# Kernel optimization log

Hardware: AMD Instinct MI355X
Metric: run time of the kernel (lower is better)

The kernel has to match this reference:

```python
import jax, jax.numpy as jnp
import numpy as np

N_NODES = 50000

def setup_inputs() -> dict:
    key = jax.random.key(0)
    k1, k2, k3, k4, k5 = jax.random.split(key, 5)
    x = jax.random.normal(k1, (50000, 512), dtype=jnp.float32)
    edge_row = jax.random.randint(k2, (800000,), 0, N_NODES, dtype=jnp.int64)
    edge_col = jax.random.randint(k3, (800000,), 0, N_NODES, dtype=jnp.int64)
    edge_val = jax.random.uniform(k4, (800000,), dtype=jnp.float32)
    # init like torch: uniform(-stdv, stdv), stdv = 1/sqrt(out_features)
    stdv = 1.0 / np.sqrt(96.0)
    weight = jax.random.uniform(k5, (512, 96), minval=-stdv, maxval=stdv, dtype=jnp.float32)
    return {"x": x, "edge_row": edge_row, "edge_col": edge_col, "edge_val": edge_val, "weight": weight}

def reference(x, edge_row, edge_col, edge_val, weight):
    # support = X @ W  -- dense GEMM [N, F_in] x [F_in, F_out]
    support = x @ weight
    # sparse adjacency matmul: out[row] += val * support[col]
    msgs = edge_val[:, None] * support[edge_col]          # [E, F_out]
    out = jax.ops.segment_sum(msgs, edge_row, num_segments=N_NODES)
    # act = ReLU (module default); bias=False
    return jax.nn.relu(out)
```

## Files before the change

### kernel.cpp

```cpp
#include <hip/hip_runtime.h>

#define N_NODES 50000
#define F_IN    512
#define F_OUT   96
#define N_EDGES 800000

#define RPB    128
#define NBKT   391
#define CAP    2560
#define ECHUNK 4096
#define NCHUNK ((N_EDGES + ECHUNK - 1) / ECHUNK)
#define GEMM_BLOCKS ((N_NODES + 63) / 64)

typedef __attribute__((ext_vector_type(8))) short bf16x8;
typedef __attribute__((ext_vector_type(4))) float f32x4;

typedef const __attribute__((address_space(1))) void* gas_ptr;
typedef __attribute__((address_space(3))) void* las_ptr;

__device__ __forceinline__ void gload_lds16(const void* g, void* l) {
    __builtin_amdgcn_global_load_lds((gas_ptr)g, (las_ptr)l, 16, 0, 0);
}

__device__ __forceinline__ unsigned short f2bf(float f) {
    unsigned int u = __float_as_uint(f);
    unsigned int r = (u + 0x7FFFu + ((u >> 16) & 1u)) >> 16;
    return (unsigned short)r;
}
__device__ __forceinline__ float bf2f(unsigned short h) {
    return __uint_as_float(((unsigned int)h) << 16);
}

__global__ __launch_bounds__(256) void k_wcast(const float* __restrict__ w,
                                               unsigned short* __restrict__ wTp,
                                               int* __restrict__ bcnt) {
    if (blockIdx.x == 0) {
        const int t = threadIdx.x;
        bcnt[t] = 0;
        if (t < 144) bcnt[256 + t] = 0;
    }
    const int i = blockIdx.x * 256 + threadIdx.x;
    if (i < F_OUT * F_IN) {
        const int n  = i >> 9;
        const int k  = i & 511;
        const int p  = k >> 6;
        const int kk = k & 63;
        const int slot = kk ^ ((n & 7) << 3);
        wTp[p * (F_OUT * 64) + n * 64 + slot] = f2bf(w[(size_t)k * F_OUT + n]);
    }
}

__global__ __launch_bounds__(256) void k_fused(const float* __restrict__ x,
                                               const unsigned short* __restrict__ wTp,
                                               unsigned short* __restrict__ support,
                                               const int* __restrict__ erow,
                                               const int* __restrict__ ecol,
                                               const float* __restrict__ eval,
                                               int* __restrict__ bcnt,
                                               float2* __restrict__ bucket) {
    __shared__ __align__(16) char smem[49152];
    const int tid = threadIdx.x;

    if (blockIdx.x < NCHUNK) {
        int* hist  = (int*)smem;
        int* gbase = hist + 400;
        int* lcur  = gbase + 400;
        for (int i = tid; i < NBKT; i += 256) { hist[i] = 0; lcur[i] = 0; }
        __syncthreads();

        const int base = blockIdx.x * ECHUNK;
        const int n = min(ECHUNK, N_EDGES - base);

        for (int i = tid; i < n; i += 256)
            atomicAdd(&hist[erow[base + i] >> 7], 1);
        __syncthreads();

        for (int b = tid; b < NBKT; b += 256)
            gbase[b] = hist[b] ? atomicAdd(&bcnt[b], hist[b]) : 0;
        __syncthreads();

        for (int i = tid; i < n; i += 256) {
            const int r = erow[base + i];
            const int b = r >> 7;
            const int pos = gbase[b] + atomicAdd(&lcur[b], 1);
            if (pos >= 0 && pos < CAP)
                bucket[(size_t)b * CAP + pos] = make_float2(
                    __int_as_float(((r & 127) << 16) | ecol[base + i]),
                    eval[base + i]);
        }
        return;
    }

    unsigned short* sB = (unsigned short*)smem;

    const int lane = tid & 63;
    const int wave = tid >> 6;
    const int r0   = (blockIdx.x - NCHUNK) * 64;
    const int lr   = lane & 15;
    const int kg   = lane >> 4;

    int grow = r0 + wave * 16 + lr;
    if (grow > N_NODES - 1) grow = N_NODES - 1;
    const float* xrow = x + (size_t)grow * F_IN + kg * 8;

    f32x4 acc[6];
    #pragma unroll
    for (int t = 0; t < 6; ++t) acc[t] = (f32x4){0.f, 0.f, 0.f, 0.f};

    float4 ar[8][4];

    auto BSTAGE = [&](int half) {
        const unsigned short* src = wTp + (size_t)half * (4 * F_OUT * 64);
        #pragma unroll
        for (int i = 0; i < 12; ++i) {
            const int chunk = i * 256 + tid;
            gload_lds16(src + chunk * 8, sB + chunk * 8);
        }
    };
    auto XLOAD = [&](int p) {
        const float* b = xrow + p * 64;
        ar[p][0] = *reinterpret_cast<const float4*>(b);
        ar[p][1] = *reinterpret_cast<const float4*>(b + 4);
        ar[p][2] = *reinterpret_cast<const float4*>(b + 32);
        ar[p][3] = *reinterpret_cast<const float4*>(b + 36);
    };
    auto COMPUTE = [&](int p) {
        const char* bb = (const char*)(sB + (p & 3) * (F_OUT * 64));
        #pragma unroll
        for (int ks = 0; ks < 2; ++ks) {
            const float4 a0 = ar[p][ks * 2];
            const float4 a1 = ar[p][ks * 2 + 1];
            bf16x8 af;
            af[0] = (short)f2bf(a0.x); af[1] = (short)f2bf(a0.y);
            af[2] = (short)f2bf(a0.z); af[3] = (short)f2bf(a0.w);
            af[4] = (short)f2bf(a1.x); af[5] = (short)f2bf(a1.y);
            af[6] = (short)f2bf(a1.z); af[7] = (short)f2bf(a1.w);
            #pragma unroll
            for (int t = 0; t < 6; ++t) {
                const int n    = t * 16 + lr;
                const int boff = (ks * 64 + kg * 16) ^ ((n & 7) << 4);
                const bf16x8 bfr = *reinterpret_cast<const bf16x8*>(bb + n * 128 + boff);
                acc[t] = __builtin_amdgcn_mfma_f32_16x16x32_bf16(af, bfr, acc[t], 0, 0, 0);
            }
        }
    };

    BSTAGE(0);
    __syncthreads();
    XLOAD(0); XLOAD(1); XLOAD(2);
    COMPUTE(0); XLOAD(3);
    COMPUTE(1); XLOAD(4);
    COMPUTE(2); XLOAD(5);
    COMPUTE(3);
    __syncthreads();
    BSTAGE(1);
    __syncthreads();
    XLOAD(6);
    COMPUTE(4); XLOAD(7);
    COMPUTE(5);
    COMPUTE(6);
    COMPUTE(7);

    #pragma unroll
    for (int t = 0; t < 6; ++t) {
        #pragma unroll
        for (int r = 0; r < 4; ++r) {
            const int row = r0 + wave * 16 + kg * 4 + r;
            if (row < N_NODES)
                support[(size_t)row * F_OUT + t * 16 + lr] = f2bf(acc[t][r]);
        }
    }
}

__global__ __launch_bounds__(256) void kS_sort(const int* __restrict__ bcnt,
                                               const float2* __restrict__ bucket,
                                               float2* __restrict__ bucket2,
                                               int* __restrict__ rowOffs) {
    __shared__ int cnt[RPB];
    __shared__ int sc[RPB];
    __shared__ int rbase[RPB];
    __shared__ int rcur[RPB];
    const int b   = blockIdx.x;
    const int tid = threadIdx.x;

    if (tid < RPB) { cnt[tid] = 0; rcur[tid] = 0; }
    __syncthreads();

    const int beg = b * CAP;
    const int n   = min(bcnt[b], CAP);

    for (int i = tid; i < n; i += 256)
        atomicAdd(&cnt[(__float_as_int(bucket[beg + i].x) >> 16) & 127], 1);
    __syncthreads();

    if (tid < RPB) sc[tid] = cnt[tid];
    __syncthreads();
    #pragma unroll
    for (int off = 1; off < RPB; off <<= 1) {
        int a = 0;
        if (tid < RPB && tid >= off) a = sc[tid - off];
        __syncthreads();
        if (tid < RPB) sc[tid] += a;
        __syncthreads();
    }
    if (tid < RPB) {
        const int rb = beg + sc[tid] - cnt[tid];
        rbase[tid] = rb;
        rowOffs[b * 129 + tid] = rb;
    }
    if (tid == RPB) rowOffs[b * 129 + RPB] = beg + n;
    __syncthreads();

    for (int i = tid; i < n; i += 256) {
        const float2 ev  = bucket[beg + i];
        const int    key = __float_as_int(ev.x);
        const int    r   = (key >> 16) & 127;
        const int    pos = rbase[r] + atomicAdd(&rcur[r], 1);
        bucket2[pos] = make_float2(__int_as_float(key & 0xFFFF), ev.y);
    }
}

__global__ __launch_bounds__(256) void k_gather(const int* __restrict__ rowOffs,
                                                const float2* __restrict__ bucket2,
                                                const unsigned short* __restrict__ support,
                                                float* __restrict__ out) {
    const int gid = blockIdx.x * 256 + threadIdx.x;
    if (gid >= N_NODES * 6) return;
    const int r   = gid / 6;
    const int f16 = gid - r * 6;

    const int idx = (r >> 7) * 129 + (r & 127);
    const int beg = rowOffs[idx];
    const int end = rowOffs[idx + 1];

    float acc[16];
    #pragma unroll
    for (int j = 0; j < 16; ++j) acc[j] = 0.f;

    for (int i = beg; i < end; ++i) {
        const float2 cv = bucket2[i];
        const int   c = __float_as_int(cv.x);
        const float v = cv.y;
        const unsigned short* sp = support + (size_t)c * F_OUT + f16 * 16;
        const bf16x8 s0 = *reinterpret_cast<const bf16x8*>(sp);
        const bf16x8 s1 = *reinterpret_cast<const bf16x8*>(sp + 8);
        #pragma unroll
        for (int j = 0; j < 8; ++j) {
            acc[j]     = fmaf(v, bf2f((unsigned short)s0[j]), acc[j]);
            acc[8 + j] = fmaf(v, bf2f((unsigned short)s1[j]), acc[8 + j]);
        }
    }

    float* o = out + (size_t)r * F_OUT + f16 * 16;
    #pragma unroll
    for (int q = 0; q < 4; ++q) {
        float4 ov;
        ov.x = fmaxf(acc[q * 4 + 0], 0.f);
        ov.y = fmaxf(acc[q * 4 + 1], 0.f);
        ov.z = fmaxf(acc[q * 4 + 2], 0.f);
        ov.w = fmaxf(acc[q * 4 + 3], 0.f);
        *reinterpret_cast<float4*>(o + q * 4) = ov;
    }
}

extern "C" void kernel_launch(void* const* d_in, const int* in_sizes, int n_in,
                              void* d_out, int out_size, void* d_ws, size_t ws_size,
                              hipStream_t stream) {
    const float* x    = (const float*)d_in[0];
    const int*   erow = (const int*)d_in[1];
    const int*   ecol = (const int*)d_in[2];
    const float* eval = (const float*)d_in[3];
    const float* w    = (const float*)d_in[4];
    float*       out  = (float*)d_out;

    unsigned short* support = (unsigned short*)d_ws;
    int*    bcnt    = (int*)((char*)d_ws + 9600000);
    int*    rowOffs = bcnt + 400;
    unsigned short* wTp = (unsigned short*)(rowOffs + 50560);
    float2* bucket  = (float2*)((char*)wTp + 98304);
    float2* bucket2 = bucket + (size_t)NBKT * CAP;

    k_wcast<<<(F_OUT * F_IN + 255) / 256, 256, 0, stream>>>(w, wTp, bcnt);

    k_fused<<<NCHUNK + GEMM_BLOCKS, 256, 0, stream>>>(x, wTp, support,
                                                      erow, ecol, eval,
                                                      bcnt, bucket);

    kS_sort<<<NBKT, 256, 0, stream>>>(bcnt, bucket, bucket2, rowOffs);

    const int gthreads = N_NODES * 6;
    k_gather<<<(gthreads + 255) / 256, 256, 0, stream>>>(rowOffs, bucket2, support, out);
}
```

Before: 83.72 us.

## Double-buffer weight tiles in LDS with explicit vmcnt waits in GEMM

Splits the staged weight tile into two 24KB LDS regions, each holding two k-panels, so later weight panels stream in while earlier ones are being consumed. X loads now go through inline-asm global loads, and the code waits on explicit s_waitcnt vmcnt counts plus raw s_barrier instead of full __syncthreads. The aim is to overlap weight staging and X loads with MFMA compute and to remove the full drain between the two halves. The hand-counted vmcnt values are fragile: a wrong count could read stale LDS or registers.

```diff
diff --git a/kernel.cpp b/kernel.cpp
--- a/kernel.cpp
+++ b/kernel.cpp
@@ -21,6 +21,18 @@
 __device__ __forceinline__ void gload_lds16(const void* g, void* l) {
     __builtin_amdgcn_global_load_lds((gas_ptr)g, (las_ptr)l, 16, 0, 0);
 }
+
+__device__ __forceinline__ float4 gload4(const float* p) {
+    float4 r;
+    asm volatile("global_load_dwordx4 %0, %1, off"
+                 : "=v"(r) : "v"(p) : "memory");
+    return r;
+}
+
+#define VMCNT_SB(n) do { \
+    asm volatile("s_waitcnt vmcnt(" #n ")" ::: "memory"); \
+    __builtin_amdgcn_sched_barrier(0); \
+} while (0)
 
 __device__ __forceinline__ unsigned short f2bf(float f) {
     unsigned int u = __float_as_uint(f);
@@ -91,8 +103,6 @@
         return;
     }
 
-    unsigned short* sB = (unsigned short*)smem;
-
     const int lane = tid & 63;
     const int wave = tid >> 6;
     const int r0   = (blockIdx.x - NCHUNK) * 64;
@@ -107,25 +117,27 @@
     #pragma unroll
     for (int t = 0; t < 6; ++t) acc[t] = (f32x4){0.f, 0.f, 0.f, 0.f};
 
+    auto BSTAGE = [&](int reg, int pair) {
+        const unsigned short* src = wTp + (size_t)pair * (2 * F_OUT * 64);
+        char* dst = smem + reg * 24576;
+        #pragma unroll
+        for (int i = 0; i < 6; ++i) {
+            const int chunk = i * 256 + tid;
+            gload_lds16(src + chunk * 8, dst + chunk * 16);
+        }
+    };
+
     float4 ar[8][4];
 
-    auto BSTAGE = [&](int half) {
-        const unsigned short* src = wTp + (size_t)half * (4 * F_OUT * 64);
-        #pragma unroll
-        for (int i = 0; i < 12; ++i) {
-            const int chunk = i * 256 + tid;
-            gload_lds16(src + chunk * 8, sB + chunk * 8);
-        }
-    };
     auto XLOAD = [&](int p) {
         const float* b = xrow + p * 64;
-        ar[p][0] = *reinterpret_cast<const float4*>(b);
-        ar[p][1] = *reinterpret_cast<const float4*>(b + 4);
-        ar[p][2] = *reinterpret_cast<const float4*>(b + 32);
-        ar[p][3] = *reinterpret_cast<const float4*>(b + 36);
+        ar[p][0] = gload4(b);
+        ar[p][1] = gload4(b + 4);
+        ar[p][2] = gload4(b + 32);
+        ar[p][3] = gload4(b + 36);
     };
     auto COMPUTE = [&](int p) {
-        const char* bb = (const char*)(sB + (p & 3) * (F_OUT * 64));
+        const char* bb = smem + (((p >> 1) & 1) * 24576) + ((p & 1) * 12288);
         #pragma unroll
         for (int ks = 0; ks < 2; ++ks) {
             const float4 a0 = ar[p][ks * 2];
@@ -145,19 +157,25 @@
         }
     };
 
-    BSTAGE(0);
-    __syncthreads();
-    XLOAD(0); XLOAD(1); XLOAD(2);
-    COMPUTE(0); XLOAD(3);
-    COMPUTE(1); XLOAD(4);
-    COMPUTE(2); XLOAD(5);
-    COMPUTE(3);
-    __syncthreads();
-    BSTAGE(1);
-    __syncthreads();
-    XLOAD(6);
-    COMPUTE(4); XLOAD(7);
+    BSTAGE(0, 0);
+    BSTAGE(1, 1);
+    XLOAD(0); XLOAD(1); XLOAD(2); XLOAD(3);
+    VMCNT_SB(16);
+    __builtin_amdgcn_s_barrier();
+
+    VMCNT_SB(12); COMPUTE(0); XLOAD(4);
+    VMCNT_SB(12); COMPUTE(1); XLOAD(5);
+    __builtin_amdgcn_s_barrier();
+    BSTAGE(0, 2);
+    VMCNT_SB(18); COMPUTE(2); XLOAD(6);
+    VMCNT_SB(18); COMPUTE(3); XLOAD(7);
+    VMCNT_SB(8);
+    __builtin_amdgcn_s_barrier();
+    BSTAGE(1, 3);
+    COMPUTE(4);
     COMPUTE(5);
+    VMCNT_SB(0);
+    __builtin_amdgcn_s_barrier();
     COMPUTE(6);
     COMPUTE(7);
 
```

New measurement: 82.33 us. About the same (-1.7%).
